# Kernel optimization log

Hardware: AMD Instinct MI355X
Metric: run time of the kernel (lower is better)

The kernel has to match this reference:

```python
import jax, jax.numpy as jnp
import numpy as np

B, L, NS = 8192, 64, 4096  # batch, n_labels, n_legal_states


def setup_inputs() -> dict:
    key = jax.random.key(0)
    k1, k2, k3, k4 = jax.random.split(key, 4)
    f = jax.random.normal(k1, (B, L), dtype=jnp.float32)
    y = (jax.random.uniform(k2, (B, L)) < 0.5).astype(jnp.float32)      # binary targets
    mask = (jax.random.uniform(k3, (B, L)) < 0.9).astype(jnp.float32)   # label mask
    S = (jax.random.uniform(k4, (NS, L)) < 0.5).astype(jnp.float32)     # legal_state indicator matrix
    return {"f": f, "y": y, "mask": mask, "S": S}


def reference(f, y, mask, S):
    # partition-function GEMM: potential[s, b] = sum_l S[s, l] * f[b, l]
    potential = S @ f.T                          # [NS, B]
    max_sf = jnp.max(potential, axis=0)          # [B]
    J = jnp.exp(potential - max_sf)              # [NS, B], stable exp-normalize
    z = jnp.sum(J, axis=0)                       # [B]
    # masked segment-reduce: pMargin[b, l] = sum_{s: S[s,l]>0} J[s, b] / z[b]
    ind = (S > 0).astype(f.dtype)                # [NS, L]
    pMargin = (ind.T @ J / z).T                  # [B, L]
    # BCELoss(reduction='none') with torch's log clamp at -100, masked, mean per sample
    logp = jnp.maximum(jnp.log(pMargin), -100.0)
    log1mp = jnp.maximum(jnp.log1p(-pMargin), -100.0)
    bce = -(y * logp + (1.0 - y) * log1mp) * mask  # [B, L]
    loss = jnp.mean(jnp.mean(bce, axis=1))
    return loss, pMargin
```

## Files before the change

### kernel.cpp

```cpp
#include <hip/hip_runtime.h>
#include <stdint.h>

#define BTOT 8192
#define NSS  4096
#define LL   64
#define BT   32
#define STT  32
#define NT   (NSS/STT)
#define NSPLIT 4
#define TPS  (NT/NSPLIT)
#define JROWB 80

typedef __bf16    bf16x8 __attribute__((ext_vector_type(8)));
typedef _Float16  f16x8  __attribute__((ext_vector_type(8)));
typedef float     f32x4  __attribute__((ext_vector_type(4)));

static __device__ __forceinline__ unsigned short f2bf(float x){
  union { float f; uint32_t u; } v; v.f = x;
  uint32_t r = v.u + 0x7fffu + ((v.u >> 16) & 1u);
  return (unsigned short)(r >> 16);
}

__global__ void prepack_kernel(const float* __restrict__ S,
                               _Float16* __restrict__ Sp,
                               unsigned short* __restrict__ STp){
  const int t = blockIdx.x;
  const int sbase = t * STT;
  #pragma unroll
  for (int rep = 0; rep < 2; ++rep){
    int item = rep * 256 + threadIdx.x;
    int frag = item >> 6;
    int lane = item & 63;
    int c16 = lane & 15, q4 = lane >> 4;
    if (frag < 4){
      int ss = frag >> 1, kc = frag & 1;
      const float* row = S + (size_t)(sbase + ss*16 + c16)*LL + kc*32 + q4*8;
      f16x8 h;
      #pragma unroll
      for (int j = 0; j < 8; ++j) h[j] = (_Float16)row[j];
      *(f16x8*)&Sp[((size_t)(t*4 + frag)*64 + lane)*8] = h;
    } else {
      int lt = frag - 4;
      int l  = lt*16 + c16;
      int s0 = sbase + q4*8;
      union { unsigned short u[8]; bf16x8 v; } H;
      #pragma unroll
      for (int j = 0; j < 8; ++j) H.u[j] = f2bf(S[(size_t)(s0 + j)*LL + l]);
      *(bf16x8*)&STp[((size_t)(t*4 + lt)*64 + lane)*8] = H.v;
    }
  }
}

__launch_bounds__(256, 4)
__global__ void fused_kernel(const float* __restrict__ f,
                             const _Float16* __restrict__ Sp,
                             const unsigned short* __restrict__ STp,
                             float* __restrict__ numPart,
                             float* __restrict__ zPart){
  const int tid  = threadIdx.x;
  const int w    = tid >> 6;
  const int lane = tid & 63;
  const int c16  = lane & 15;
  const int q4   = lane >> 4;
  const int bt   = blockIdx.x & 255;
  const int sp   = blockIdx.x >> 8;
  const int bb   = bt * BT;

  __shared__ unsigned char jraw[4][32 * JROWB];
  __shared__ float nredQ[4][16 * 33];
  __shared__ float zred[4][128];

  f16x8 fB[2][2];
  #pragma unroll
  for (int g = 0; g < 2; ++g){
    const float* frow = f + (size_t)(bb + g*16 + c16) * LL;
    #pragma unroll
    for (int kc = 0; kc < 2; ++kc){
      float vv[8];
      *(float4*)&vv[0] = *(const float4*)&frow[kc*32 + 8*q4];
      *(float4*)&vv[4] = *(const float4*)&frow[kc*32 + 8*q4 + 4];
      f16x8 h;
      #pragma unroll
      for (int j = 0; j < 8; ++j) h[j] = (_Float16)vv[j];
      fB[g][kc] = h;
    }
  }

  f32x4 acc2[4][2];
  #pragma unroll
  for (int lt = 0; lt < 4; ++lt)
    #pragma unroll
    for (int g = 0; g < 2; ++g) acc2[lt][g] = (f32x4){0.f,0.f,0.f,0.f};
  float zpart[2] = {0.f, 0.f};

  unsigned char* jb = jraw[w];

#define LOAD_A1(TT, A1) do {                                              \
    const _Float16* ps_ = Sp + ((size_t)((TT)*4)*64 + lane)*8;            \
    _Pragma("unroll")                                                     \
    for (int k_ = 0; k_ < 4; ++k_)                                        \
      (A1)[k_] = *(const f16x8*)(ps_ + (size_t)k_*64*8);                  \
  } while(0)

#define COMPUTE_TILE(TT, A1) do {                                         \
               \
    bf16x8 a2_[4];                                                        \
    const unsigned short* pt_ = STp + ((size_t)((TT)*4)*64 + lane)*8;     \
    _Pragma("unroll")                                                     \
    for (int lt_ = 0; lt_ < 4; ++lt_)                                     \
      a2_[lt_] = *(const bf16x8*)(pt_ + (size_t)lt_*64*8);                \
                                         \
    f32x4 p_[2][2];                                                       \
    _Pragma("unroll")                                                     \
    for (int ss_ = 0; ss_ < 2; ++ss_)                                     \
      _Pragma("unroll")                                                   \
      for (int g_ = 0; g_ < 2; ++g_){                                     \
        f32x4 a_ = (f32x4){0.f,0.f,0.f,0.f};                              \
        a_ = __builtin_amdgcn_mfma_f32_16x16x32_f16((A1)[ss_*2+0], fB[g_][0], a_, 0,0,0); \
        a_ = __builtin_amdgcn_mfma_f32_16x16x32_f16((A1)[ss_*2+1], fB[g_][1], a_, 0,0,0); \
        p_[ss_][g_] = a_;                                                 \
      }                                                                   \
                               \
    _Pragma("unroll")                                                     \
    for (int ss_ = 0; ss_ < 2; ++ss_)                                     \
      _Pragma("unroll")                                                   \
      for (int g_ = 0; g_ < 2; ++g_){                                     \
        float J0 = __expf(p_[ss_][g_][0]);                                \
        float J1 = __expf(p_[ss_][g_][1]);                                \
        float J2 = __expf(p_[ss_][g_][2]);                                \
        float J3 = __expf(p_[ss_][g_][3]);                                \
        zpart[g_] += (J0 + J1) + (J2 + J3);                               \
        union { __bf16 h[4]; uint2 u2; } P_;                              \
        P_.h[0] = (__bf16)J0; P_.h[1] = (__bf16)J1;                       \
        P_.h[2] = (__bf16)J2; P_.h[3] = (__bf16)J3;                       \
        *(uint2*)&jb[(g_*16 + c16)*JROWB + ss_*32 + q4*8] = P_.u2;        \
      }                                                                   \
                               \
    bf16x8 b2_[2];                                                        \
    _Pragma("unroll")                                                     \
    for (int g_ = 0; g_ < 2; ++g_)                                        \
      b2_[g_] = *(const bf16x8*)&jb[(g_*16 + c16)*JROWB + q4*16];         \
                                        \
    _Pragma("unroll")                                                     \
    for (int lt_ = 0; lt_ < 4; ++lt_)                                     \
      _Pragma("unroll")                                                   \
      for (int g_ = 0; g_ < 2; ++g_)                                      \
        acc2[lt_][g_] = __builtin_amdgcn_mfma_f32_16x16x32_bf16(a2_[lt_], b2_[g_], acc2[lt_][g_], 0,0,0); \
  } while(0)

  const int tb = sp * TPS + w * 8;
  f16x8 a1A[4], a1B[4];
  LOAD_A1(tb+0, a1A);
  LOAD_A1(tb+1, a1B);  COMPUTE_TILE(tb+0, a1A);
  LOAD_A1(tb+2, a1A);  COMPUTE_TILE(tb+1, a1B);
  LOAD_A1(tb+3, a1B);  COMPUTE_TILE(tb+2, a1A);
  LOAD_A1(tb+4, a1A);  COMPUTE_TILE(tb+3, a1B);
  LOAD_A1(tb+5, a1B);  COMPUTE_TILE(tb+4, a1A);
  LOAD_A1(tb+6, a1A);  COMPUTE_TILE(tb+5, a1B);
  LOAD_A1(tb+7, a1B);  COMPUTE_TILE(tb+6, a1A);
  COMPUTE_TILE(tb+7, a1B);

#undef LOAD_A1
#undef COMPUTE_TILE

  float* numOut = numPart + (size_t)sp * BTOT * LL + (size_t)bb * LL;
  zred[w][q4*32 + c16]      = zpart[0];
  zred[w][q4*32 + 16 + c16] = zpart[1];

  #pragma unroll
  for (int lt = 0; lt < 4; ++lt){
    #pragma unroll
    for (int g = 0; g < 2; ++g)
      #pragma unroll
      for (int jj = 0; jj < 4; ++jj)
        nredQ[w][(q4*4 + jj)*33 + g*16 + c16] = acc2[lt][g][jj];
    __syncthreads();
    if (lt == 0 && tid < BT){
      float zz = 0.f;
      #pragma unroll
      for (int ww = 0; ww < 4; ++ww)
        #pragma unroll
        for (int qq = 0; qq < 4; ++qq) zz += zred[ww][qq*32 + tid];
      zPart[(size_t)sp * BTOT + bb + tid] = zz;
    }
    #pragma unroll
    for (int it = 0; it < 2; ++it){
      int idx = it*256 + tid;
      int b = idx >> 4, l = idx & 15;
      float v = (nredQ[0][l*33+b] + nredQ[1][l*33+b]) + (nredQ[2][l*33+b] + nredQ[3][l*33+b]);
      numOut[(size_t)b*LL + lt*16 + l] = v;
    }
    __syncthreads();
  }
}

__global__ void finalize_kernel(const float* __restrict__ numPart,
                                const float* __restrict__ zPart,
                                const float* __restrict__ y,
                                const float* __restrict__ mask,
                                float* __restrict__ out,
                                float* __restrict__ parts){
  int tid = threadIdx.x;
  int idx = blockIdx.x * 256 + tid;
  int b = idx >> 6;
  float num = 0.f, z = 0.f;
  #pragma unroll
  for (int sp = 0; sp < NSPLIT; ++sp){
    num += numPart[(size_t)sp * BTOT * LL + idx];
    z   += zPart[(size_t)sp * BTOT + b];
  }
  float p = fminf(num / z, 1.0f);
  out[1 + idx] = p;
  float lg = fmaxf(__logf(p), -100.f);
  float l1 = fmaxf(log1pf(-p), -100.f);
  float yv = y[idx], mv = mask[idx];
  float lsum = -(yv*lg + (1.f - yv)*l1) * mv;
  #pragma unroll
  for (int off = 32; off; off >>= 1) lsum += __shfl_down(lsum, off);
  __shared__ float wred[4];
  int w = tid >> 6, lane = tid & 63;
  if (lane == 0) wred[w] = lsum;
  __syncthreads();
  if (tid == 0) parts[blockIdx.x] = (wred[0] + wred[1]) + (wred[2] + wred[3]);
}

__global__ void loss_kernel(const float* __restrict__ parts, float* __restrict__ out){
  float v = 0.f;
  #pragma unroll
  for (int i = 0; i < 8; ++i) v += parts[threadIdx.x + 256*i];
  #pragma unroll
  for (int off = 32; off; off >>= 1) v += __shfl_down(v, off);
  __shared__ float sred[4];
  int w = threadIdx.x >> 6, lane = threadIdx.x & 63;
  if (lane == 0) sred[w] = v;
  __syncthreads();
  if (threadIdx.x == 0)
    out[0] = ((sred[0] + sred[1]) + (sred[2] + sred[3])) * (1.0f / ((float)BTOT * (float)LL));
}

extern "C" void kernel_launch(void* const* d_in, const int* in_sizes, int n_in,
                              void* d_out, int out_size, void* d_ws, size_t ws_size,
                              hipStream_t stream){
  const float* f = (const float*)d_in[0];
  const float* y = (const float*)d_in[1];
  const float* m = (const float*)d_in[2];
  const float* S = (const float*)d_in[3];
  float* out = (float*)d_out;

  _Float16* Sp        = (_Float16*)d_ws;
  unsigned short* STp = (unsigned short*)(Sp + (size_t)NT*4*64*8);
  char* p = (char*)d_ws + (size_t)2 * NT * 4 * 64 * 8 * 2;
  float* numPart = (float*)p;  p += (size_t)NSPLIT * BTOT * LL * sizeof(float);
  float* zPart   = (float*)p;  p += (size_t)NSPLIT * BTOT * sizeof(float);
  float* parts   = (float*)p;

  prepack_kernel<<<NT, 256, 0, stream>>>(S, Sp, STp);
  fused_kernel<<<256 * NSPLIT, 256, 0, stream>>>(f, Sp, STp, numPart, zPart);
  finalize_kernel<<<(BTOT*LL)/256, 256, 0, stream>>>(numPart, zPart, y, m, out, parts);
  loss_kernel<<<1, 256, 0, stream>>>(parts, out);
}
```

Baseline: 35.88 us.

## Software-pipeline exp stage with second GEMM using double-buffered per-warp LDS

Restructures the per-warp tile loop so the second (bf16) GEMM for tile t-1 runs after the exp/pack of tile t, using two LDS J buffers per warp. The first GEMM's A operand is prefetched one tile ahead, and the ST operand is loaded a tile early. The reduction scratch arrays are aliased onto the enlarged J buffer, with a barrier added before they are reused. The goal is to hide the LDS write-to-read latency and the exp latency behind MFMA work. In exchange it doubles LDS per warp and raises register pressure, which could reduce occupancy.

Result: no change. 35.75 us (-0.4%).

```diff
diff --git a/kernel.cpp b/kernel.cpp
--- a/kernel.cpp
+++ b/kernel.cpp
@@ -10,6 +10,7 @@
 #define NSPLIT 4
 #define TPS  (NT/NSPLIT)
 #define JROWB 80
+#define JBUFB (32 * JROWB)
 
 typedef __bf16    bf16x8 __attribute__((ext_vector_type(8)));
 typedef _Float16  f16x8  __attribute__((ext_vector_type(8)));
@@ -66,9 +67,10 @@
   const int sp   = blockIdx.x >> 8;
   const int bb   = bt * BT;
 
-  __shared__ unsigned char jraw[4][32 * JROWB];
-  __shared__ float nredQ[4][16 * 33];
-  __shared__ float zred[4][128];
+  __shared__ unsigned char smem[4 * 2 * JBUFB];
+  unsigned char* jraw = smem + w * 2 * JBUFB;
+  float (*nredQ)[16*33] = (float (*)[16*33])smem;
+  float (*zred)[128]    = (float (*)[128])(smem + 4*528*4);
 
   f16x8 fB[2][2];
   #pragma unroll
@@ -93,75 +95,87 @@
     for (int g = 0; g < 2; ++g) acc2[lt][g] = (f32x4){0.f,0.f,0.f,0.f};
   float zpart[2] = {0.f, 0.f};
 
-  unsigned char* jb = jraw[w];
-
-#define LOAD_A1(TT, A1) do {                                              \
-    const _Float16* ps_ = Sp + ((size_t)((TT)*4)*64 + lane)*8;            \
-    _Pragma("unroll")                                                     \
-    for (int k_ = 0; k_ < 4; ++k_)                                        \
-      (A1)[k_] = *(const f16x8*)(ps_ + (size_t)k_*64*8);                  \
-  } while(0)
-
-#define COMPUTE_TILE(TT, A1) do {                                         \
-               \
-    bf16x8 a2_[4];                                                        \
-    const unsigned short* pt_ = STp + ((size_t)((TT)*4)*64 + lane)*8;     \
-    _Pragma("unroll")                                                     \
-    for (int lt_ = 0; lt_ < 4; ++lt_)                                     \
-      a2_[lt_] = *(const bf16x8*)(pt_ + (size_t)lt_*64*8);                \
-                                         \
-    f32x4 p_[2][2];                                                       \
-    _Pragma("unroll")                                                     \
-    for (int ss_ = 0; ss_ < 2; ++ss_)                                     \
-      _Pragma("unroll")                                                   \
-      for (int g_ = 0; g_ < 2; ++g_){                                     \
-        f32x4 a_ = (f32x4){0.f,0.f,0.f,0.f};                              \
-        a_ = __builtin_amdgcn_mfma_f32_16x16x32_f16((A1)[ss_*2+0], fB[g_][0], a_, 0,0,0); \
-        a_ = __builtin_amdgcn_mfma_f32_16x16x32_f16((A1)[ss_*2+1], fB[g_][1], a_, 0,0,0); \
-        p_[ss_][g_] = a_;                                                 \
-      }                                                                   \
-                               \
-    _Pragma("unroll")                                                     \
-    for (int ss_ = 0; ss_ < 2; ++ss_)                                     \
-      _Pragma("unroll")                                                   \
-      for (int g_ = 0; g_ < 2; ++g_){                                     \
-        float J0 = __expf(p_[ss_][g_][0]);                                \
-        float J1 = __expf(p_[ss_][g_][1]);                                \
-        float J2 = __expf(p_[ss_][g_][2]);                                \
-        float J3 = __expf(p_[ss_][g_][3]);                                \
-        zpart[g_] += (J0 + J1) + (J2 + J3);                               \
-        union { __bf16 h[4]; uint2 u2; } P_;                              \
-        P_.h[0] = (__bf16)J0; P_.h[1] = (__bf16)J1;                       \
-        P_.h[2] = (__bf16)J2; P_.h[3] = (__bf16)J3;                       \
-        *(uint2*)&jb[(g_*16 + c16)*JROWB + ss_*32 + q4*8] = P_.u2;        \
-      }                                                                   \
-                               \
-    bf16x8 b2_[2];                                                        \
-    _Pragma("unroll")                                                     \
-    for (int g_ = 0; g_ < 2; ++g_)                                        \
-      b2_[g_] = *(const bf16x8*)&jb[(g_*16 + c16)*JROWB + q4*16];         \
-                                        \
-    _Pragma("unroll")                                                     \
-    for (int lt_ = 0; lt_ < 4; ++lt_)                                     \
-      _Pragma("unroll")                                                   \
-      for (int g_ = 0; g_ < 2; ++g_)                                      \
-        acc2[lt_][g_] = __builtin_amdgcn_mfma_f32_16x16x32_bf16(a2_[lt_], b2_[g_], acc2[lt_][g_], 0,0,0); \
-  } while(0)
-
   const int tb = sp * TPS + w * 8;
-  f16x8 a1A[4], a1B[4];
-  LOAD_A1(tb+0, a1A);
-  LOAD_A1(tb+1, a1B);  COMPUTE_TILE(tb+0, a1A);
-  LOAD_A1(tb+2, a1A);  COMPUTE_TILE(tb+1, a1B);
-  LOAD_A1(tb+3, a1B);  COMPUTE_TILE(tb+2, a1A);
-  LOAD_A1(tb+4, a1A);  COMPUTE_TILE(tb+3, a1B);
-  LOAD_A1(tb+5, a1B);  COMPUTE_TILE(tb+4, a1A);
-  LOAD_A1(tb+6, a1A);  COMPUTE_TILE(tb+5, a1B);
-  LOAD_A1(tb+7, a1B);  COMPUTE_TILE(tb+6, a1A);
-  COMPUTE_TILE(tb+7, a1B);
-
-#undef LOAD_A1
-#undef COMPUTE_TILE
+  f16x8  a1[2][4];
+  bf16x8 a2[2][4];
+  {
+    const _Float16* ps = Sp + ((size_t)(tb*4)*64 + lane)*8;
+    #pragma unroll
+    for (int k = 0; k < 4; ++k) a1[0][k] = *(const f16x8*)(ps + (size_t)k*64*8);
+  }
+
+  #pragma unroll
+  for (int t = 0; t < 8; ++t){
+    const int cur = t & 1, nxt = cur ^ 1;
+    unsigned char* jcur = jraw + cur * JBUFB;
+    unsigned char* jprv = jraw + nxt * JBUFB;
+
+    f32x4 p_[2][2];
+    #pragma unroll
+    for (int ss = 0; ss < 2; ++ss)
+      #pragma unroll
+      for (int g = 0; g < 2; ++g){
+        f32x4 a = (f32x4){0.f,0.f,0.f,0.f};
+        a = __builtin_amdgcn_mfma_f32_16x16x32_f16(a1[cur][ss*2+0], fB[g][0], a, 0,0,0);
+        a = __builtin_amdgcn_mfma_f32_16x16x32_f16(a1[cur][ss*2+1], fB[g][1], a, 0,0,0);
+        p_[ss][g] = a;
+      }
+
+    if (t < 7){
+      const _Float16* ps = Sp + ((size_t)((tb+t+1)*4)*64 + lane)*8;
+      #pragma unroll
+      for (int k = 0; k < 4; ++k) a1[nxt][k] = *(const f16x8*)(ps + (size_t)k*64*8);
+    }
+
+    #pragma unroll
+    for (int ss = 0; ss < 2; ++ss)
+      #pragma unroll
+      for (int g = 0; g < 2; ++g){
+        float J0 = __expf(p_[ss][g][0]);
+        float J1 = __expf(p_[ss][g][1]);
+        float J2 = __expf(p_[ss][g][2]);
+        float J3 = __expf(p_[ss][g][3]);
+        zpart[g] += (J0 + J1) + (J2 + J3);
+        union { __bf16 h[4]; uint2 u2; } P_;
+        P_.h[0] = (__bf16)J0; P_.h[1] = (__bf16)J1;
+        P_.h[2] = (__bf16)J2; P_.h[3] = (__bf16)J3;
+        *(uint2*)&jcur[(g*16 + c16)*JROWB + ss*32 + q4*8] = P_.u2;
+      }
+
+    if (t > 0){
+      bf16x8 b2[2];
+      #pragma unroll
+      for (int g = 0; g < 2; ++g)
+        b2[g] = *(const bf16x8*)&jprv[(g*16 + c16)*JROWB + q4*16];
+      #pragma unroll
+      for (int lt = 0; lt < 4; ++lt)
+        #pragma unroll
+        for (int g = 0; g < 2; ++g)
+          acc2[lt][g] = __builtin_amdgcn_mfma_f32_16x16x32_bf16(a2[nxt][lt], b2[g], acc2[lt][g], 0,0,0);
+    }
+
+    {
+      const unsigned short* pt = STp + ((size_t)((tb+t)*4)*64 + lane)*8;
+      #pragma unroll
+      for (int lt = 0; lt < 4; ++lt)
+        a2[cur][lt] = *(const bf16x8*)(pt + (size_t)lt*64*8);
+    }
+  }
+
+  {
+    unsigned char* jprv = jraw + 1 * JBUFB;
+    bf16x8 b2[2];
+    #pragma unroll
+    for (int g = 0; g < 2; ++g)
+      b2[g] = *(const bf16x8*)&jprv[(g*16 + c16)*JROWB + q4*16];
+    #pragma unroll
+    for (int lt = 0; lt < 4; ++lt)
+      #pragma unroll
+      for (int g = 0; g < 2; ++g)
+        acc2[lt][g] = __builtin_amdgcn_mfma_f32_16x16x32_bf16(a2[1][lt], b2[g], acc2[lt][g], 0,0,0);
+  }
+
+  __syncthreads();
 
   float* numOut = numPart + (size_t)sp * BTOT * LL + (size_t)bb * LL;
   zred[w][q4*32 + c16]      = zpart[0];
```
